# Kernel tuning notes

Measured on AMD Instinct MI355X. Metric: run time of the kernel, lower is better.

## Reference

```python
import jax, jax.numpy as jnp
import numpy as np

B, C, H, W = 4, 256, 224, 224
WH = WW = 8
SH = SW = 4
HEADS = 8
HD = C // HEADS
N = WH * WW
EPS = 1e-5


def _rel_index():
    coords = np.stack(np.meshgrid(np.arange(WH), np.arange(WW), indexing='ij')).reshape(2, -1)
    rel = (coords[:, :, None] - coords[:, None, :]).transpose(1, 2, 0).copy()
    rel[:, :, 0] += WH - 1
    rel[:, :, 1] += WW - 1
    rel[:, :, 0] *= 2 * WW - 1
    return rel.sum(-1)  # (N, N) int

REL_INDEX = _rel_index()


def _shift_mask(Hp, Wp):
    # Swin shift mask for one image: (nW, N, N) float, 0 or -100
    img = np.zeros((Hp, Wp))
    cnt = 0
    for a, b in [(0, Hp - WH), (Hp - WH, Hp - SH), (Hp - SH, Hp)]:
        for c, d in [(0, Wp - WW), (Wp - WW, Wp - SW), (Wp - SW, Wp)]:
            img[a:b, c:d] = cnt
            cnt += 1
    mw = img.reshape(Hp // WH, WH, Wp // WW, WW).transpose(0, 2, 1, 3).reshape(-1, N)
    diff = mw[:, None, :] - mw[:, :, None]  # [w, i, j] = mw[w,j] - mw[w,i]
    return np.where(diff != 0, np.float32(-100.0), np.float32(0.0)).astype(np.float32)


def _ln(x, w, b):
    m = jnp.mean(x, axis=-1, keepdims=True)
    v = jnp.mean(jnp.square(x - m), axis=-1, keepdims=True)
    return (x - m) * jax.lax.rsqrt(v + EPS) * w + b


def setup_inputs() -> dict:
    key = jax.random.key(0)
    ks = jax.random.split(key, 8)
    num_rel = (2 * WH - 1) * (2 * WW - 1)
    return {
        'x': jax.random.normal(ks[0], (B, C, H, W), dtype=jnp.float32),
        'qkv_w': jax.random.normal(ks[1], (3 * C, C), dtype=jnp.float32) * 0.02,
        'proj_w': jax.random.normal(ks[2], (C, C), dtype=jnp.float32) * 0.02,
        'proj_b': jnp.zeros((C,), dtype=jnp.float32),
        'rpb_table': jax.random.normal(ks[3], (num_rel, HEADS), dtype=jnp.float32) * 0.02,
        'norm1_w': jnp.ones((C,), dtype=jnp.float32),
        'norm1_b': jnp.zeros((C,), dtype=jnp.float32),
        'norm2_w': jnp.ones((C,), dtype=jnp.float32),
        'norm2_b': jnp.zeros((C,), dtype=jnp.float32),
        'mlp_w1': jax.random.normal(ks[4], (4 * C, C), dtype=jnp.float32) * 0.02,
        'mlp_b1': jnp.zeros((4 * C,), dtype=jnp.float32),
        'mlp_w2': jax.random.normal(ks[5], (C, 4 * C), dtype=jnp.float32) * 0.02,
        'mlp_b2': jnp.zeros((C,), dtype=jnp.float32),
    }


def reference(x, qkv_w, proj_w, proj_b, rpb_table, norm1_w, norm1_b,
              norm2_w, norm2_b, mlp_w1, mlp_b1, mlp_w2, mlp_b2):
    Bx, Cx, Hx, Wx = x.shape
    pad_h = (WH - Hx % WH) % WH
    pad_w = (WW - Wx % WW) % WW
    if pad_h or pad_w:
        x = jnp.pad(x, ((0, 0), (0, 0), (0, pad_h), (0, pad_w)))
    Hp, Wp = Hx + pad_h, Wx + pad_w
    x = jnp.transpose(x, (0, 2, 3, 1))                    # BHWC
    x = jnp.roll(x, (-SH, -SW), axis=(1, 2))
    nW = (Hp // WH) * (Wp // WW)
    # window partition -> (B*nW, N, C), batch-major
    xw = x.reshape(Bx, Hp // WH, WH, Wp // WW, WW, Cx)
    xw = jnp.transpose(xw, (0, 1, 3, 2, 4, 5)).reshape(-1, N, Cx)

    # ----- windowed attention -----
    h = _ln(xw, norm1_w, norm1_b)
    qkv = (h @ qkv_w.T).reshape(-1, N, 3, HEADS, HD)
    qkv = jnp.transpose(qkv, (2, 0, 3, 1, 4))             # (3, Bw, heads, N, hd)
    q, k, v = qkv[0], qkv[1], qkv[2]
    attn = jnp.einsum('bhnd,bhmd->bhnm', q, k) * (1.0 / HD ** 0.5)
    bias = jnp.transpose(rpb_table[REL_INDEX.reshape(-1)].reshape(N, N, HEADS), (2, 0, 1))
    attn = attn + bias[None]
    # faithful to torch: repeat_interleave(B, dim=0) -> window-major mask ordering
    mask = jnp.asarray(_shift_mask(Hp, Wp))               # (nW, N, N)
    attn = attn + jnp.repeat(mask, Bx, axis=0)[:, None]
    attn = jax.nn.softmax(attn, axis=-1)
    out = jnp.einsum('bhnm,bhmd->bhnd', attn, v)
    out = jnp.transpose(out, (0, 2, 1, 3)).reshape(-1, N, Cx)
    out = out @ proj_w.T + proj_b
    xw = xw + out

    # ----- MLP -----
    h = _ln(xw, norm2_w, norm2_b)
    h = jax.nn.gelu(h @ mlp_w1.T + mlp_b1, approximate=False) @ mlp_w2.T + mlp_b2
    xw = xw + h

    # window reverse, un-shift, un-pad
    x = xw.reshape(Bx, Hp // WH, Wp // WW, WH, WW, Cx)
    x = jnp.transpose(x, (0, 1, 3, 2, 4, 5)).reshape(Bx, Hp, Wp, Cx)
    x = jnp.roll(x, (SH, SW), axis=(1, 2))
    x = x[:, :Hx, :Wx, :]
    return jnp.transpose(x, (0, 3, 1, 2))
```

## Files before the change

kernel.cpp:

```cpp
#include <hip/hip_runtime.h>

typedef unsigned short u16;
typedef unsigned int   u32;
typedef __attribute__((ext_vector_type(8))) __bf16 bf16x8;
typedef __attribute__((ext_vector_type(4))) float  f32x4;
typedef __attribute__((ext_vector_type(4))) u16    u16x4;
typedef __attribute__((ext_vector_type(8))) u16    u16x8;

#define DEV __device__ __forceinline__

DEV u16 f2b(float f) {
  union { float f; u32 u; } a; a.f = f;
  const u32 u = a.u;
  return (u16)((u + 0x7fffu + ((u >> 16) & 1u)) >> 16);
}

DEV float gelu_fast(float x) {
  const float x2 = x * x;
  const float t  = __builtin_fmaf(0.1029430f, x2, 2.3022150f);
  const float e  = __builtin_exp2f(x * t);
  const float r  = __builtin_amdgcn_rcpf(1.0f + e);
  return __builtin_fmaf(-x, r, x);
}

DEV void gload16(const void* g, void* l) {
  __builtin_amdgcn_global_load_lds(
      (const __attribute__((address_space(1))) void*)g,
      (__attribute__((address_space(3))) void*)l, 16, 0, 0);
}

__global__ __launch_bounds__(256)
void conv_weights(const float* __restrict__ qkvw, const float* __restrict__ projw,
                  const float* __restrict__ w1,   const float* __restrict__ w2,
                  u16* __restrict__ dq, u16* __restrict__ dp,
                  u16* __restrict__ d1, u16* __restrict__ d2) {
  const int t = blockIdx.x * 256 + threadIdx.x;
  if (t < 196608)      dq[t]          = f2b(qkvw[t]);
  else if (t < 262144) dp[t - 196608] = f2b(projw[t - 196608]);
  else if (t < 524288) d1[t - 262144] = f2b(w1[t - 262144]);
  else                 d2[t - 524288] = f2b(w2[t - 524288]);
}

__global__ __launch_bounds__(256)
void ln1_win(const float* __restrict__ x, const float* __restrict__ w1,
             const float* __restrict__ b1, u16* __restrict__ hout,
             float* __restrict__ xwout) {
  __shared__ float xt[64 * 257];
  __shared__ float smean[256], srstd[256];
  const int tid = threadIdx.x, lane = tid & 63, wv = tid >> 6;
  const int g = blockIdx.x;
  const int b = g / 196, rem = g % 196;
  const int wh = rem / 7, wg = rem % 7;
  const int base_r = b * 784 + wh * 28 + wg * 4;
  const int pr = tid >> 5, pc = tid & 31;
  int hp = wh * 8 + 4 + pr; if (hp >= 224) hp -= 224;
  int wp = wg * 32 + 4 + pc; if (wp >= 224) wp -= 224;
  const long roff = (long)b * 256 * 50176 + hp * 224 + wp;

  float s = 0.f, q = 0.f;
  for (int cc = 0; cc < 4; ++cc) {
#pragma unroll 8
    for (int i = 0; i < 64; ++i) {
      const int c = cc * 64 + i;
      const float v = x[(long)c * 50176 + roff];
      xt[i * 257 + tid] = v;
      s += v; q += v * v;
    }
    __syncthreads();
#pragma unroll 8
    for (int jj = 0; jj < 64; ++jj) {
      const int p = jj * 4 + wv;
      const int m = (base_r + ((p & 31) >> 3)) * 64 + (p >> 5) * 8 + (p & 7);
      xwout[(long)m * 256 + cc * 64 + lane] = xt[lane * 257 + p];
    }
    __syncthreads();
  }
  const float mean = s * (1.f / 256.f);
  smean[tid] = mean;
  srstd[tid] = rsqrtf(q * (1.f / 256.f) - mean * mean + 1e-5f);
  __syncthreads();

  float wr_[4], br_[4];
#pragma unroll
  for (int cc = 0; cc < 4; ++cc) { wr_[cc] = w1[cc * 64 + lane]; br_[cc] = b1[cc * 64 + lane]; }
#pragma unroll 2
  for (int jj = 0; jj < 64; ++jj) {
    const int p = jj * 4 + wv;
    const int m = (base_r + ((p & 31) >> 3)) * 64 + (p >> 5) * 8 + (p & 7);
    const float mu = smean[p], rs = srstd[p];
#pragma unroll
    for (int cc = 0; cc < 4; ++cc) {
      const float v = xwout[(long)m * 256 + cc * 64 + lane];
      hout[(long)m * 256 + cc * 64 + lane] = f2b((v - mu) * rs * wr_[cc] + br_[cc]);
    }
  }
}

template<int EPI, int NCOL>
__global__ __launch_bounds__(512, 4)
void gemm_bt(const u16* __restrict__ A, const u16* __restrict__ Bw, const int K,
             float* __restrict__ fout, const float* __restrict__ bias,
             u16* __restrict__ bout,
             const float* __restrict__ lnw, const float* __restrict__ lnb,
             float* __restrict__ oout) {
  __shared__ __align__(16) u16 smem[24576];
  u16* sA0 = smem;
  u16* sB0 = smem + 4096;
  u16* sA1 = smem + 12288;
  u16* sB1 = smem + 16384;

  const int tid  = threadIdx.x;
  const int lane = tid & 63;
  const int wid  = tid >> 6;
  const int wrr  = wid >> 2;
  const int wcc  = wid & 3;

  const int nwg = gridDim.x;
  const int bid = blockIdx.x;
  const int wg  = (bid & 7) * (nwg >> 3) + (bid >> 3);
  const int row_blk = wg / NCOL;
  const int col_blk = wg - row_blk * NCOL;
  const int row0 = row_blk * 128;
  const int col0 = col_blk * 256;

  const f32x4 vzero = {0.f, 0.f, 0.f, 0.f};
  f32x4 acc[4][4];
#pragma unroll
  for (int i = 0; i < 4; ++i)
#pragma unroll
    for (int j = 0; j < 4; ++j) acc[i][j] = vzero;

  const int l15  = lane & 15;
  const int l4   = lane >> 4;
  const int ksw2 = (l15 >> 1) & 3;
  const int lcol = (((tid & 3) ^ ((tid >> 3) & 3)) << 3);

  const u16* pA  = A  + (long)(row0 + (tid >> 2)) * K + lcol;
  const u16* pB  = Bw + (long)(col0 + (tid >> 2)) * K + lcol;
  const u16* pB2 = pB + (long)128 * K;
  const int wbase = wid * 512;

#define STAGE_TILE(KT, DA, DB)                  \
  {                                             \
    gload16(pA  + (KT), (DA) + wbase);          \
    gload16(pB  + (KT), (DB) + wbase);          \
    gload16(pB2 + (KT), (DB) + 4096 + wbase);   \
  }

#define COMPUTE_TILE(SA, SB, SWAP)                                                      \
  {                                                                                     \
    bf16x8 af[4], bfv[4];                                                               \
    _Pragma("unroll")                                                                   \
    for (int mi = 0; mi < 4; ++mi)                                                      \
      af[mi] = *(const bf16x8*)((SA) + (wrr * 64 + mi * 16 + l15) * 32 +                \
                                ((l4 ^ ksw2) << 3));                                    \
    _Pragma("unroll")                                                                   \
    for (int nj = 0; nj < 4; ++nj)                                                      \
      bfv[nj] = *(const bf16x8*)((SB) + (wcc * 64 + nj * 16 + l15) * 32 +               \
                                 ((l4 ^ ksw2) << 3));                                   \
    _Pragma("unroll")                                                                   \
    for (int mi = 0; mi < 4; ++mi)                                                      \
      _Pragma("unroll")                                                                 \
      for (int nj = 0; nj < 4; ++nj) {                                                  \
        if (SWAP)                                                                       \
          acc[mi][nj] = __builtin_amdgcn_mfma_f32_16x16x32_bf16(bfv[nj], af[mi],        \
                                                                acc[mi][nj], 0, 0, 0);  \
        else                                                                            \
          acc[mi][nj] = __builtin_amdgcn_mfma_f32_16x16x32_bf16(af[mi], bfv[nj],        \
                                                                acc[mi][nj], 0, 0, 0);  \
      }                                                                                 \
  }

#define KLOOP(SWAP)                                                  \
  {                                                                  \
    const int nt = K >> 5;                                           \
    STAGE_TILE(0, sA0, sB0);                                         \
    int cur = 0;                                                     \
    for (int t = 0; t < nt; ++t) {                                   \
      u16* cA = cur ? sA1 : sA0;                                     \
      u16* cB = cur ? sB1 : sB0;                                     \
      u16* nA = cur ? sA0 : sA1;                                     \
      u16* nB = cur ? sB0 : sB1;                                     \
      if (t + 1 < nt) {                                              \
        STAGE_TILE((t + 1) << 5, nA, nB);                            \
        asm volatile("s_waitcnt vmcnt(3)" ::: "memory");             \
      } else {                                                       \
        asm volatile("s_waitcnt vmcnt(0)" ::: "memory");             \
      }                                                              \
      __builtin_amdgcn_s_barrier();                                  \
      asm volatile("" ::: "memory");                                 \
      COMPUTE_TILE(cA, cB, SWAP);                                    \
      asm volatile("" ::: "memory");                                 \
      __builtin_amdgcn_s_barrier();                                  \
      cur ^= 1;                                                      \
    }                                                                \
  }

  if (EPI == 0 && col_blk == 2) {
    KLOOP(0);
#pragma unroll
    for (int mi = 0; mi < 4; ++mi) {
      const int mb = row0 + wrr * 64 + mi * 16 + (l4 << 2);
      const int rrg = mb >> 6, ii = mb & 63;
#pragma unroll
      for (int nj = 0; nj < 4; ++nj) {
        const int n = 512 + wcc * 64 + nj * 16 + l15;
        const int hh = (n >> 5) & 7, d = n & 31;
        u16x4 p;
#pragma unroll
        for (int reg = 0; reg < 4; ++reg) p[reg] = f2b(acc[mi][nj][reg]);
        *(u16x4*)(bout + 102760448L + (long)((rrg * 8 + hh) * 32 + d) * 64 + ii) = p;
      }
    }
    return;
  }

  KLOOP(1);

#undef STAGE_TILE
#undef COMPUTE_TILE
#undef KLOOP

  if (EPI == 0) {
#pragma unroll
    for (int mi = 0; mi < 4; ++mi) {
      const int m = row0 + wrr * 64 + mi * 16 + l15;
      const int rr = m >> 6, ii = m & 63;
#pragma unroll
      for (int nj = 0; nj < 4; ++nj) {
        const int n = col0 + wcc * 64 + nj * 16 + (l4 << 2);
        const int s = n >> 8, hh = (n >> 5) & 7, d = n & 31;
        u16x4 p;
#pragma unroll
        for (int reg = 0; reg < 4; ++reg) p[reg] = f2b(acc[mi][nj][reg]);
        *(u16x4*)(bout + (long)s * 51380224L +
                  (long)((rr * 8 + hh) * 64 + ii) * 32 + d) = p;
      }
    }
  } else if (EPI == 1) {
    f32x4 b4[4];
#pragma unroll
    for (int nj = 0; nj < 4; ++nj)
      b4[nj] = *(const f32x4*)(bias + wcc * 64 + nj * 16 + (l4 << 2));
    float sS[4], sQ[4];
#pragma unroll
    for (int mi = 0; mi < 4; ++mi) {
      const int m = row0 + wrr * 64 + mi * 16 + l15;
      float* yrow = fout + (long)m * 256;
      float s = 0.f, q = 0.f;
#pragma unroll
      for (int nj = 0; nj < 4; ++nj) {
        const int n = wcc * 64 + nj * 16 + (l4 << 2);
        f32x4 o = *(f32x4*)(yrow + n);
#pragma unroll
        for (int reg = 0; reg < 4; ++reg) {
          o[reg] += acc[mi][nj][reg] + b4[nj][reg];
          s += o[reg]; q += o[reg] * o[reg];
        }
        *(f32x4*)(yrow + n) = o;
        acc[mi][nj] = o;
      }
      s += __shfl_xor(s, 16); s += __shfl_xor(s, 32);
      q += __shfl_xor(q, 16); q += __shfl_xor(q, 32);
      sS[mi] = s; sQ[mi] = q;
    }
    float* ps = (float*)smem;
    float* pq = ps + 512;
    __syncthreads();
    if (lane < 16) {
#pragma unroll
      for (int mi = 0; mi < 4; ++mi) {
        const int idx = (wrr * 64 + mi * 16 + l15) * 4 + wcc;
        ps[idx] = sS[mi]; pq[idx] = sQ[mi];
      }
    }
    __syncthreads();
#pragma unroll
    for (int mi = 0; mi < 4; ++mi) {
      const int m = row0 + wrr * 64 + mi * 16 + l15;
      const int base = (wrr * 64 + mi * 16 + l15) * 4;
      const float S = ps[base] + ps[base + 1] + ps[base + 2] + ps[base + 3];
      const float Q = pq[base] + pq[base + 1] + pq[base + 2] + pq[base + 3];
      const float mean = S * (1.f / 256.f);
      const float rstd = rsqrtf(Q * (1.f / 256.f) - mean * mean + 1e-5f);
#pragma unroll
      for (int nj = 0; nj < 4; ++nj) {
        const int n = wcc * 64 + nj * 16 + (l4 << 2);
        const f32x4 w4 = *(const f32x4*)(lnw + n);
        const f32x4 c4 = *(const f32x4*)(lnb + n);
        u16x4 p;
#pragma unroll
        for (int reg = 0; reg < 4; ++reg)
          p[reg] = f2b((acc[mi][nj][reg] - mean) * rstd * w4[reg] + c4[reg]);
        *(u16x4*)(bout + (long)m * 256 + n) = p;
      }
    }
  } else if (EPI == 3) {
    f32x4 b4[4];
#pragma unroll
    for (int nj = 0; nj < 4; ++nj)
      b4[nj] = *(const f32x4*)(bias + wcc * 64 + nj * 16 + (l4 << 2));
#pragma unroll
    for (int mi = 0; mi < 4; ++mi) {
      const int m = row0 + wrr * 64 + mi * 16 + l15;
      const float* yrow = fout + (long)m * 256;
#pragma unroll
      for (int nj = 0; nj < 4; ++nj) {
        const int n = wcc * 64 + nj * 16 + (l4 << 2);
        const f32x4 yv = *(const f32x4*)(yrow + n);
#pragma unroll
        for (int reg = 0; reg < 4; ++reg)
          acc[mi][nj][reg] += yv[reg] + b4[nj][reg];
      }
    }
    const int wr0 = row0 >> 6;
    const int b = wr0 / 784, rem = wr0 % 784;
    const int wh = rem / 28, wwb = rem % 28;
    float* tp = (float*)smem;
    const int pidx = tid & 127, cgrp = tid >> 7;
    const int pr = pidx >> 4, pc = pidx & 15;
    int hp = wh * 8 + 4 + pr;  if (hp >= 224) hp -= 224;
    int wp = wwb * 8 + 4 + pc; if (wp >= 224) wp -= 224;
    float* ob = oout + (long)b * 256 * 50176 + hp * 224 + wp;
#pragma unroll
    for (int cc = 0; cc < 4; ++cc) {
      __syncthreads();
      if (wcc == cc) {
#pragma unroll
        for (int mi = 0; mi < 4; ++mi) {
          const int ml = wrr * 64 + mi * 16 + l15;
          const int px = ((ml & 63) >> 3) * 16 + (ml >> 6) * 8 + (ml & 7);
#pragma unroll
          for (int nj = 0; nj < 4; ++nj)
#pragma unroll
            for (int reg = 0; reg < 4; ++reg)
              tp[(nj * 16 + (l4 << 2) + reg) * 128 + (px ^ (l4 << 2))] =
                  acc[mi][nj][reg];
        }
      }
      __syncthreads();
#pragma unroll 4
      for (int j = 0; j < 16; ++j) {
        const int cl = cgrp * 16 + j;
        ob[(long)(cc * 64 + cl) * 50176] =
            tp[cl * 128 + (pidx ^ (((cl >> 2) & 3) << 2))];
      }
    }
  } else if (EPI == 2) {
    f32x4 b4[4];
#pragma unroll
    for (int nj = 0; nj < 4; ++nj)
      b4[nj] = *(const f32x4*)(bias + col0 + wcc * 64 + nj * 16 + (l4 << 2));
#pragma unroll
    for (int mi = 0; mi < 4; ++mi) {
      const int m = row0 + wrr * 64 + mi * 16 + l15;
#pragma unroll
      for (int nj = 0; nj < 4; ++nj) {
        const int n = col0 + wcc * 64 + nj * 16 + (l4 << 2);
        u16x4 p;
#pragma unroll
        for (int reg = 0; reg < 4; ++reg)
          p[reg] = f2b(gelu_fast(acc[mi][nj][reg] + b4[nj][reg]));
        *(u16x4*)(bout + (long)m * 1024 + n) = p;
      }
    }
  }
}

__global__ __launch_bounds__(256)
void attn_win(const u16* __restrict__ qkv, const float* __restrict__ rpb,
              u16* __restrict__ aout) {
  __shared__ u16 Pl[4][4096];
  __shared__ float srpb[1800];
  const int tid = threadIdx.x, lane = tid & 63, wv = tid >> 6;
  const int bid = blockIdx.x;
  const int r = bid >> 1;
  const int h = (bid & 1) * 4 + wv;
  for (int i = tid; i < 1800; i += 256) srpb[i] = rpb[i];
  __syncthreads();

  const int midx = r >> 2;
  const int wh = midx / 28, ww = midx % 28;
  const int l15 = lane & 15, l4 = lane >> 4;

  u16* Pw = &Pl[wv][0];
  const long hb = (long)(r * 8 + h) * 2048;
  const u16* qh = qkv + hb;
  const u16* kh = qkv + 51380224 + hb;
  const u16* vh = qkv + 102760448 + hb;

  int rj[4], cj[4], labj[4];
#pragma unroll
  for (int nj = 0; nj < 4; ++nj) {
    const int j = nj * 16 + l15;
    rj[nj] = j >> 3; cj[nj] = j & 7;
    const int hp = wh * 8 + rj[nj], wp = ww * 8 + cj[nj];
    const int lh = (hp < 216) ? 0 : ((hp < 220) ? 1 : 2);
    const int lw = (wp < 216) ? 0 : ((wp < 220) ? 1 : 2);
    labj[nj] = lh * 3 + lw;
  }

  const f32x4 vzero = {0.f, 0.f, 0.f, 0.f};

  bf16x8 qf[4], kf[4];
#pragma unroll
  for (int mi = 0; mi < 4; ++mi)
    qf[mi] = *(const bf16x8*)(qh + (mi * 16 + l15) * 32 + l4 * 8);
#pragma unroll
  for (int nj = 0; nj < 4; ++nj)
    kf[nj] = *(const bf16x8*)(kh + (nj * 16 + l15) * 32 + l4 * 8);

  f32x4 S[4][4];
#pragma unroll
  for (int mi = 0; mi < 4; ++mi)
#pragma unroll
    for (int nj = 0; nj < 4; ++nj)
      S[mi][nj] = __builtin_amdgcn_mfma_f32_16x16x32_bf16(qf[mi], kf[nj], vzero, 0, 0, 0);

#pragma unroll
  for (int mi = 0; mi < 4; ++mi)
#pragma unroll
    for (int reg = 0; reg < 4; ++reg) {
      const int i = mi * 16 + (l4 << 2) + reg;
      const int ri = i >> 3, ci = i & 7;
      const int hp = wh * 8 + ri, wp = ww * 8 + ci;
      const int lh = (hp < 216) ? 0 : ((hp < 220) ? 1 : 2);
      const int lw = (wp < 216) ? 0 : ((wp < 220) ? 1 : 2);
      const int li = lh * 3 + lw;
      float v[4];
#pragma unroll
      for (int nj = 0; nj < 4; ++nj) {
        const int idx = (ri - rj[nj] + 7) * 15 + (ci - cj[nj] + 7);
        v[nj] = S[mi][nj][reg] * 0.17677669529663687f + srpb[idx * 8 + h]
              + ((li != labj[nj]) ? -100.0f : 0.0f);
      }
      float mx = fmaxf(fmaxf(v[0], v[1]), fmaxf(v[2], v[3]));
      mx = fmaxf(mx, __shfl_xor(mx, 1));
      mx = fmaxf(mx, __shfl_xor(mx, 2));
      mx = fmaxf(mx, __shfl_xor(mx, 4));
      mx = fmaxf(mx, __shfl_xor(mx, 8));
      float sum = 0.f;
#pragma unroll
      for (int nj = 0; nj < 4; ++nj) { v[nj] = __expf(v[nj] - mx); sum += v[nj]; }
      sum += __shfl_xor(sum, 1);
      sum += __shfl_xor(sum, 2);
      sum += __shfl_xor(sum, 4);
      sum += __shfl_xor(sum, 8);
      const float rinv = __builtin_amdgcn_rcpf(sum);
      const int sw = (i & 7) << 3;
#pragma unroll
      for (int nj = 0; nj < 4; ++nj)
        Pw[i * 64 + ((nj * 16 + l15) ^ sw)] = f2b(v[nj] * rinv);
    }

  f32x4 OT[2][4];
#pragma unroll
  for (int td = 0; td < 2; ++td)
#pragma unroll
    for (int ti = 0; ti < 4; ++ti) OT[td][ti] = vzero;

  const int rsw = (l15 & 7) << 3;
#pragma unroll
  for (int kk = 0; kk < 2; ++kk) {
    bf16x8 pf[4], vf[2];
#pragma unroll
    for (int ti = 0; ti < 4; ++ti)
      pf[ti] = *(const bf16x8*)(Pw + (ti * 16 + l15) * 64 + ((kk * 32 + l4 * 8) ^ rsw));
#pragma unroll
    for (int td = 0; td < 2; ++td)
      vf[td] = *(const bf16x8*)(vh + (td * 16 + l15) * 64 + kk * 32 + l4 * 8);
#pragma unroll
    for (int td = 0; td < 2; ++td)
#pragma unroll
      for (int ti = 0; ti < 4; ++ti)
        OT[td][ti] = __builtin_amdgcn_mfma_f32_16x16x32_bf16(vf[td], pf[ti], OT[td][ti], 0, 0, 0);
  }

#pragma unroll
  for (int td = 0; td < 2; ++td)
#pragma unroll
    for (int ti = 0; ti < 4; ++ti) {
      const int i = ti * 16 + l15;
      const int d0 = td * 16 + (l4 << 2);
      u16x4 p;
#pragma unroll
      for (int reg = 0; reg < 4; ++reg) p[reg] = f2b(OT[td][ti][reg]);
      *(u16x4*)(aout + (long)(r * 64 + i) * 256 + h * 32 + d0) = p;
    }
}

extern "C" void kernel_launch(void* const* d_in, const int* in_sizes, int n_in,
                              void* d_out, int out_size, void* d_ws, size_t ws_size,
                              hipStream_t stream) {
  (void)in_sizes; (void)n_in; (void)out_size; (void)ws_size;
  const float* x     = (const float*)d_in[0];
  const float* qkvw  = (const float*)d_in[1];
  const float* projw = (const float*)d_in[2];
  const float* projb = (const float*)d_in[3];
  const float* rpb   = (const float*)d_in[4];
  const float* n1w   = (const float*)d_in[5];
  const float* n1b   = (const float*)d_in[6];
  const float* n2w   = (const float*)d_in[7];
  const float* n2b   = (const float*)d_in[8];
  const float* w1    = (const float*)d_in[9];
  const float* b1    = (const float*)d_in[10];
  const float* w2    = (const float*)d_in[11];
  const float* b2    = (const float*)d_in[12];

  char* ws = (char*)d_ws;
  u16*   hbuf   = (u16*)(ws);
  u16*   qkvb   = (u16*)(ws + 102760448);
  u16*   abuf   = (u16*)(ws + 411041792);
  float* ybuf   = (float*)(ws + 513802240);
  u16*   hidb   = (u16*)(ws + 102760448);
  u16*   qkvwb  = (u16*)(ws + 719323136);
  u16*   projwb = (u16*)(ws + 719716352);
  u16*   w1b    = (u16*)(ws + 719847424);
  u16*   w2b    = (u16*)(ws + 720371712);

  conv_weights<<<3072, 256, 0, stream>>>(qkvw, projw, w1, w2, qkvwb, projwb, w1b, w2b);
  ln1_win<<<784, 256, 0, stream>>>(x, n1w, n1b, hbuf, ybuf);
  gemm_bt<0, 3><<<4704, 512, 0, stream>>>(hbuf, qkvwb, 256, nullptr, nullptr, qkvb, nullptr, nullptr, nullptr);
  attn_win<<<6272, 256, 0, stream>>>(qkvb, rpb, abuf);
  gemm_bt<1, 1><<<1568, 512, 0, stream>>>(abuf, projwb, 256, ybuf, projb, hbuf, n2w, n2b, nullptr);
  gemm_bt<2, 4><<<6272, 512, 0, stream>>>(hbuf, w1b, 256, nullptr, b1, hidb, nullptr, nullptr, nullptr);
  gemm_bt<3, 1><<<1568, 512, 0, stream>>>(hidb, w2b, 1024, ybuf, b2, nullptr, nullptr, nullptr, (float*)d_out);
}
```

Measured before the change: 1.130 ms.

## Loop over all column blocks per workgroup and use nontemporal stores

```diff
diff --git a/kernel.cpp b/kernel.cpp
--- a/kernel.cpp
+++ b/kernel.cpp
@@ -118,26 +118,16 @@
   const int nwg = gridDim.x;
   const int bid = blockIdx.x;
   const int wg  = (bid & 7) * (nwg >> 3) + (bid >> 3);
-  const int row_blk = wg / NCOL;
-  const int col_blk = wg - row_blk * NCOL;
-  const int row0 = row_blk * 128;
-  const int col0 = col_blk * 256;
+  const int row0 = wg * 128;
 
   const f32x4 vzero = {0.f, 0.f, 0.f, 0.f};
-  f32x4 acc[4][4];
-#pragma unroll
-  for (int i = 0; i < 4; ++i)
-#pragma unroll
-    for (int j = 0; j < 4; ++j) acc[i][j] = vzero;
 
   const int l15  = lane & 15;
   const int l4   = lane >> 4;
   const int ksw2 = (l15 >> 1) & 3;
   const int lcol = (((tid & 3) ^ ((tid >> 3) & 3)) << 3);
 
-  const u16* pA  = A  + (long)(row0 + (tid >> 2)) * K + lcol;
-  const u16* pB  = Bw + (long)(col0 + (tid >> 2)) * K + lcol;
-  const u16* pB2 = pB + (long)128 * K;
+  const u16* pA = A + (long)(row0 + (tid >> 2)) * K + lcol;
   const int wbase = wid * 512;
 
 #define STAGE_TILE(KT, DA, DB)                  \
@@ -196,175 +186,191 @@
     }                                                                \
   }
 
-  if (EPI == 0 && col_blk == 2) {
-    KLOOP(0);
-#pragma unroll
-    for (int mi = 0; mi < 4; ++mi) {
-      const int mb = row0 + wrr * 64 + mi * 16 + (l4 << 2);
-      const int rrg = mb >> 6, ii = mb & 63;
-#pragma unroll
-      for (int nj = 0; nj < 4; ++nj) {
-        const int n = 512 + wcc * 64 + nj * 16 + l15;
-        const int hh = (n >> 5) & 7, d = n & 31;
-        u16x4 p;
-#pragma unroll
-        for (int reg = 0; reg < 4; ++reg) p[reg] = f2b(acc[mi][nj][reg]);
-        *(u16x4*)(bout + 102760448L + (long)((rrg * 8 + hh) * 32 + d) * 64 + ii) = p;
-      }
-    }
-    return;
-  }
-
-  KLOOP(1);
+#pragma unroll
+  for (int cb = 0; cb < NCOL; ++cb) {
+    const int col0 = cb * 256;
+    const u16* pB  = Bw + (long)(col0 + (tid >> 2)) * K + lcol;
+    const u16* pB2 = pB + (long)128 * K;
+
+    f32x4 acc[4][4];
+#pragma unroll
+    for (int i = 0; i < 4; ++i)
+#pragma unroll
+      for (int j = 0; j < 4; ++j) acc[i][j] = vzero;
+
+    if (EPI == 0 && cb == 2) {
+      KLOOP(0);
+#pragma unroll
+      for (int mi = 0; mi < 4; ++mi) {
+        const int mb = row0 + wrr * 64 + mi * 16 + (l4 << 2);
+        const int rrg = mb >> 6, ii = mb & 63;
+#pragma unroll
+        for (int nj = 0; nj < 4; ++nj) {
+          const int n = 512 + wcc * 64 + nj * 16 + l15;
+          const int hh = (n >> 5) & 7, d = n & 31;
+          u16x4 p;
+#pragma unroll
+          for (int reg = 0; reg < 4; ++reg) p[reg] = f2b(acc[mi][nj][reg]);
+          __builtin_nontemporal_store(p,
+              (u16x4*)(bout + 102760448L + (long)((rrg * 8 + hh) * 32 + d) * 64 + ii));
+        }
+      }
+      continue;
+    }
+
+    KLOOP(1);
+
+    if (EPI == 0) {
+#pragma unroll
+      for (int mi = 0; mi < 4; ++mi) {
+        const int m = row0 + wrr * 64 + mi * 16 + l15;
+        const int rr = m >> 6, ii = m & 63;
+#pragma unroll
+        for (int nj = 0; nj < 4; ++nj) {
+          const int n = col0 + wcc * 64 + nj * 16 + (l4 << 2);
+          const int s = n >> 8, hh = (n >> 5) & 7, d = n & 31;
+          u16x4 p;
+#pragma unroll
+          for (int reg = 0; reg < 4; ++reg) p[reg] = f2b(acc[mi][nj][reg]);
+          __builtin_nontemporal_store(p,
+              (u16x4*)(bout + (long)s * 51380224L +
+                       (long)((rr * 8 + hh) * 64 + ii) * 32 + d));
+        }
+      }
+    } else if (EPI == 1) {
+      f32x4 b4[4];
+#pragma unroll
+      for (int nj = 0; nj < 4; ++nj)
+        b4[nj] = *(const f32x4*)(bias + wcc * 64 + nj * 16 + (l4 << 2));
+      float sS[4], sQ[4];
+#pragma unroll
+      for (int mi = 0; mi < 4; ++mi) {
+        const int m = row0 + wrr * 64 + mi * 16 + l15;
+        float* yrow = fout + (long)m * 256;
+        float s = 0.f, q = 0.f;
+#pragma unroll
+        for (int nj = 0; nj < 4; ++nj) {
+          const int n = wcc * 64 + nj * 16 + (l4 << 2);
+          f32x4 o = *(f32x4*)(yrow + n);
+#pragma unroll
+          for (int reg = 0; reg < 4; ++reg) {
+            o[reg] += acc[mi][nj][reg] + b4[nj][reg];
+            s += o[reg]; q += o[reg] * o[reg];
+          }
+          __builtin_nontemporal_store(o, (f32x4*)(yrow + n));
+          acc[mi][nj] = o;
+        }
+        s += __shfl_xor(s, 16); s += __shfl_xor(s, 32);
+        q += __shfl_xor(q, 16); q += __shfl_xor(q, 32);
+        sS[mi] = s; sQ[mi] = q;
+      }
+      float* ps = (float*)smem;
+      float* pq = ps + 512;
+      __syncthreads();
+      if (lane < 16) {
+#pragma unroll
+        for (int mi = 0; mi < 4; ++mi) {
+          const int idx = (wrr * 64 + mi * 16 + l15) * 4 + wcc;
+          ps[idx] = sS[mi]; pq[idx] = sQ[mi];
+        }
+      }
+      __syncthreads();
+#pragma unroll
+      for (int mi = 0; mi < 4; ++mi) {
+        const int m = row0 + wrr * 64 + mi * 16 + l15;
+        const int base = (wrr * 64 + mi * 16 + l15) * 4;
+        const float S = ps[base] + ps[base + 1] + ps[base + 2] + ps[base + 3];
+        const float Q = pq[base] + pq[base + 1] + pq[base + 2] + pq[base + 3];
+        const float mean = S * (1.f / 256.f);
+        const float rstd = rsqrtf(Q * (1.f / 256.f) - mean * mean + 1e-5f);
+#pragma unroll
+        for (int nj = 0; nj < 4; ++nj) {
+          const int n = wcc * 64 + nj * 16 + (l4 << 2);
+          const f32x4 w4 = *(const f32x4*)(lnw + n);
+          const f32x4 c4 = *(const f32x4*)(lnb + n);
+          u16x4 p;
+#pragma unroll
+          for (int reg = 0; reg < 4; ++reg)
+            p[reg] = f2b((acc[mi][nj][reg] - mean) * rstd * w4[reg] + c4[reg]);
+          __builtin_nontemporal_store(p, (u16x4*)(bout + (long)m * 256 + n));
+        }
+      }
+    } else if (EPI == 3) {
+      f32x4 b4[4];
+#pragma unroll
+      for (int nj = 0; nj < 4; ++nj)
+        b4[nj] = *(const f32x4*)(bias + wcc * 64 + nj * 16 + (l4 << 2));
+#pragma unroll
+      for (int mi = 0; mi < 4; ++mi) {
+        const int m = row0 + wrr * 64 + mi * 16 + l15;
+        const float* yrow = fout + (long)m * 256;
+#pragma unroll
+        for (int nj = 0; nj < 4; ++nj) {
+          const int n = wcc * 64 + nj * 16 + (l4 << 2);
+          const f32x4 yv = *(const f32x4*)(yrow + n);
+#pragma unroll
+          for (int reg = 0; reg < 4; ++reg)
+            acc[mi][nj][reg] += yv[reg] + b4[nj][reg];
+        }
+      }
+      const int wr0 = row0 >> 6;
+      const int b = wr0 / 784, rem = wr0 % 784;
+      const int wh = rem / 28, wwb = rem % 28;
+      float* tp = (float*)smem;
+      const int pidx = tid & 127, cgrp = tid >> 7;
+      const int pr = pidx >> 4, pc = pidx & 15;
+      int hp = wh * 8 + 4 + pr;  if (hp >= 224) hp -= 224;
+      int wp = wwb * 8 + 4 + pc; if (wp >= 224) wp -= 224;
+      float* ob = oout + (long)b * 256 * 50176 + hp * 224 + wp;
+#pragma unroll
+      for (int cc = 0; cc < 4; ++cc) {
+        __syncthreads();
+        if (wcc == cc) {
+#pragma unroll
+          for (int mi = 0; mi < 4; ++mi) {
+            const int ml = wrr * 64 + mi * 16 + l15;
+            const int px = ((ml & 63) >> 3) * 16 + (ml >> 6) * 8 + (ml & 7);
+#pragma unroll
+            for (int nj = 0; nj < 4; ++nj)
+#pragma unroll
+              for (int reg = 0; reg < 4; ++reg)
+                tp[(nj * 16 + (l4 << 2) + reg) * 128 + (px ^ (l4 << 2))] =
+                    acc[mi][nj][reg];
+          }
+        }
+        __syncthreads();
+#pragma unroll 4
+        for (int j = 0; j < 16; ++j) {
+          const int cl = cgrp * 16 + j;
+          __builtin_nontemporal_store(
+              tp[cl * 128 + (pidx ^ (((cl >> 2) & 3) << 2))],
+              ob + (long)(cc * 64 + cl) * 50176);
+        }
+      }
+    } else if (EPI == 2) {
+      f32x4 b4[4];
+#pragma unroll
+      for (int nj = 0; nj < 4; ++nj)
+        b4[nj] = *(const f32x4*)(bias + col0 + wcc * 64 + nj * 16 + (l4 << 2));
+#pragma unroll
+      for (int mi = 0; mi < 4; ++mi) {
+        const int m = row0 + wrr * 64 + mi * 16 + l15;
+#pragma unroll
+        for (int nj = 0; nj < 4; ++nj) {
+          const int n = col0 + wcc * 64 + nj * 16 + (l4 << 2);
+          u16x4 p;
+#pragma unroll
+          for (int reg = 0; reg < 4; ++reg)
+            p[reg] = f2b(gelu_fast(acc[mi][nj][reg] + b4[nj][reg]));
+          __builtin_nontemporal_store(p, (u16x4*)(bout + (long)m * 1024 + n));
+        }
+      }
+    }
+  }
 
 #undef STAGE_TILE
 #undef COMPUTE_TILE
 #undef KLOOP
-
-  if (EPI == 0) {
-#pragma unroll
-    for (int mi = 0; mi < 4; ++mi) {
-      const int m = row0 + wrr * 64 + mi * 16 + l15;
-      const int rr = m >> 6, ii = m & 63;
-#pragma unroll
-      for (int nj = 0; nj < 4; ++nj) {
-        const int n = col0 + wcc * 64 + nj * 16 + (l4 << 2);
-        const int s = n >> 8, hh = (n >> 5) & 7, d = n & 31;
-        u16x4 p;
-#pragma unroll
-        for (int reg = 0; reg < 4; ++reg) p[reg] = f2b(acc[mi][nj][reg]);
-        *(u16x4*)(bout + (long)s * 51380224L +
-                  (long)((rr * 8 + hh) * 64 + ii) * 32 + d) = p;
-      }
-    }
-  } else if (EPI == 1) {
-    f32x4 b4[4];
-#pragma unroll
-    for (int nj = 0; nj < 4; ++nj)
-      b4[nj] = *(const f32x4*)(bias + wcc * 64 + nj * 16 + (l4 << 2));
-    float sS[4], sQ[4];
-#pragma unroll
-    for (int mi = 0; mi < 4; ++mi) {
-      const int m = row0 + wrr * 64 + mi * 16 + l15;
-      float* yrow = fout + (long)m * 256;
-      float s = 0.f, q = 0.f;
-#pragma unroll
-      for (int nj = 0; nj < 4; ++nj) {
-        const int n = wcc * 64 + nj * 16 + (l4 << 2);
-        f32x4 o = *(f32x4*)(yrow + n);
-#pragma unroll
-        for (int reg = 0; reg < 4; ++reg) {
-          o[reg] += acc[mi][nj][reg] + b4[nj][reg];
-          s += o[reg]; q += o[reg] * o[reg];
-        }
-        *(f32x4*)(yrow + n) = o;
-        acc[mi][nj] = o;
-      }
-      s += __shfl_xor(s, 16); s += __shfl_xor(s, 32);
-      q += __shfl_xor(q, 16); q += __shfl_xor(q, 32);
-      sS[mi] = s; sQ[mi] = q;
-    }
-    float* ps = (float*)smem;
-    float* pq = ps + 512;
-    __syncthreads();
-    if (lane < 16) {
-#pragma unroll
-      for (int mi = 0; mi < 4; ++mi) {
-        const int idx = (wrr * 64 + mi * 16 + l15) * 4 + wcc;
-        ps[idx] = sS[mi]; pq[idx] = sQ[mi];
-      }
-    }
-    __syncthreads();
-#pragma unroll
-    for (int mi = 0; mi < 4; ++mi) {
-      const int m = row0 + wrr * 64 + mi * 16 + l15;
-      const int base = (wrr * 64 + mi * 16 + l15) * 4;
-      const float S = ps[base] + ps[base + 1] + ps[base + 2] + ps[base + 3];
-      const float Q = pq[base] + pq[base + 1] + pq[base + 2] + pq[base + 3];
-      const float mean = S * (1.f / 256.f);
-      const float rstd = rsqrtf(Q * (1.f / 256.f) - mean * mean + 1e-5f);
-#pragma unroll
-      for (int nj = 0; nj < 4; ++nj) {
-        const int n = wcc * 64 + nj * 16 + (l4 << 2);
-        const f32x4 w4 = *(const f32x4*)(lnw + n);
-        const f32x4 c4 = *(const f32x4*)(lnb + n);
-        u16x4 p;
-#pragma unroll
-        for (int reg = 0; reg < 4; ++reg)
-          p[reg] = f2b((acc[mi][nj][reg] - mean) * rstd * w4[reg] + c4[reg]);
-        *(u16x4*)(bout + (long)m * 256 + n) = p;
-      }
-    }
-  } else if (EPI == 3) {
-    f32x4 b4[4];
-#pragma unroll
-    for (int nj = 0; nj < 4; ++nj)
-      b4[nj] = *(const f32x4*)(bias + wcc * 64 + nj * 16 + (l4 << 2));
-#pragma unroll
-    for (int mi = 0; mi < 4; ++mi) {
-      const int m = row0 + wrr * 64 + mi * 16 + l15;
-      const float* yrow = fout + (long)m * 256;
-#pragma unroll
-      for (int nj = 0; nj < 4; ++nj) {
-        const int n = wcc * 64 + nj * 16 + (l4 << 2);
-        const f32x4 yv = *(const f32x4*)(yrow + n);
-#pragma unroll
-        for (int reg = 0; reg < 4; ++reg)
-          acc[mi][nj][reg] += yv[reg] + b4[nj][reg];
-      }
-    }
-    const int wr0 = row0 >> 6;
-    const int b = wr0 / 784, rem = wr0 % 784;
-    const int wh = rem / 28, wwb = rem % 28;
-    float* tp = (float*)smem;
-    const int pidx = tid & 127, cgrp = tid >> 7;
-    const int pr = pidx >> 4, pc = pidx & 15;
-    int hp = wh * 8 + 4 + pr;  if (hp >= 224) hp -= 224;
-    int wp = wwb * 8 + 4 + pc; if (wp >= 224) wp -= 224;
-    float* ob = oout + (long)b * 256 * 50176 + hp * 224 + wp;
-#pragma unroll
-    for (int cc = 0; cc < 4; ++cc) {
-      __syncthreads();
-      if (wcc == cc) {
-#pragma unroll
-        for (int mi = 0; mi < 4; ++mi) {
-          const int ml = wrr * 64 + mi * 16 + l15;
-          const int px = ((ml & 63) >> 3) * 16 + (ml >> 6) * 8 + (ml & 7);
-#pragma unroll
-          for (int nj = 0; nj < 4; ++nj)
-#pragma unroll
-            for (int reg = 0; reg < 4; ++reg)
-              tp[(nj * 16 + (l4 << 2) + reg) * 128 + (px ^ (l4 << 2))] =
-                  acc[mi][nj][reg];
-        }
-      }
-      __syncthreads();
-#pragma unroll 4
-      for (int j = 0; j < 16; ++j) {
-        const int cl = cgrp * 16 + j;
-        ob[(long)(cc * 64 + cl) * 50176] =
-            tp[cl * 128 + (pidx ^ (((cl >> 2) & 3) << 2))];
-      }
-    }
-  } else if (EPI == 2) {
-    f32x4 b4[4];
-#pragma unroll
-    for (int nj = 0; nj < 4; ++nj)
-      b4[nj] = *(const f32x4*)(bias + col0 + wcc * 64 + nj * 16 + (l4 << 2));
-#pragma unroll
-    for (int mi = 0; mi < 4; ++mi) {
-      const int m = row0 + wrr * 64 + mi * 16 + l15;
-#pragma unroll
-      for (int nj = 0; nj < 4; ++nj) {
-        const int n = col0 + wcc * 64 + nj * 16 + (l4 << 2);
-        u16x4 p;
-#pragma unroll
-        for (int reg = 0; reg < 4; ++reg)
-          p[reg] = f2b(gelu_fast(acc[mi][nj][reg] + b4[nj][reg]));
-        *(u16x4*)(bout + (long)m * 1024 + n) = p;
-      }
-    }
-  }
 }
 
 __global__ __launch_bounds__(256)
@@ -520,9 +526,9 @@
 
   conv_weights<<<3072, 256, 0, stream>>>(qkvw, projw, w1, w2, qkvwb, projwb, w1b, w2b);
   ln1_win<<<784, 256, 0, stream>>>(x, n1w, n1b, hbuf, ybuf);
-  gemm_bt<0, 3><<<4704, 512, 0, stream>>>(hbuf, qkvwb, 256, nullptr, nullptr, qkvb, nullptr, nullptr, nullptr);
+  gemm_bt<0, 3><<<1568, 512, 0, stream>>>(hbuf, qkvwb, 256, nullptr, nullptr, qkvb, nullptr, nullptr, nullptr);
   attn_win<<<6272, 256, 0, stream>>>(qkvb, rpb, abuf);
   gemm_bt<1, 1><<<1568, 512, 0, stream>>>(abuf, projwb, 256, ybuf, projb, hbuf, n2w, n2b, nullptr);
-  gemm_bt<2, 4><<<6272, 512, 0, stream>>>(hbuf, w1b, 256, nullptr, b1, hidb, nullptr, nullptr, nullptr);
+  gemm_bt<2, 4><<<1568, 512, 0, stream>>>(hbuf, w1b, 256, nullptr, b1, hidb, nullptr, nullptr, nullptr);
   gemm_bt<3, 1><<<1568, 512, 0, stream>>>(hidb, w2b, 1024, ybuf, b2, nullptr, nullptr, nullptr, (float*)d_out);
 }
```

Measured after the change: 1.506 ms. +33.3%, slower.
